# Performance work log

Measured on AMD Instinct MI355X. Metric: run time of the kernel, lower is better.

The kernel has to match this reference:

```python
import jax, jax.numpy as jnp
import numpy as np
import math

B = 262144
STATE = 6
TOTAL_MEAS = 27
HID = 256
INPUT_DIM = TOTAL_MEAS * 2 + 1 + STATE + 12  # 73
PI = math.pi
NORM_R_SCALE = 500.0 / 150000.0
ANG_IDX = np.array([0, 1, 3, 4, 6, 9, 10, 12, 13, 15, 18, 19, 21, 22, 24])
ANG_MASK = np.zeros((TOTAL_MEAS,), dtype=bool)
ANG_MASK[ANG_IDX] = True


def setup_inputs() -> dict:
    key = jax.random.key(0)
    ks = jax.random.split(key, 16)
    s = lambda fan: 1.0 / math.sqrt(fan)
    inp = {
        "meas": jax.random.normal(ks[0], (B, TOTAL_MEAS), jnp.float32),
        "mask": jnp.ones((B, TOTAL_MEAS), jnp.float32),
        "dt": jax.random.uniform(ks[1], (B,), jnp.float32),
        "baselines": jax.random.normal(ks[2], (B, 12), jnp.float32),
        "x_prev": jax.random.normal(ks[3], (B, STATE), jnp.float32),
        "hx": jnp.zeros((B, HID), jnp.float32),
        # GRU params (torch gate order: r, z, n)
        "W_ih": jax.random.uniform(ks[4], (3 * HID, INPUT_DIM), jnp.float32, -s(HID), s(HID)),
        "W_hh": jax.random.uniform(ks[5], (3 * HID, HID), jnp.float32, -s(HID), s(HID)),
        "b_ih": jax.random.uniform(ks[6], (3 * HID,), jnp.float32, -s(HID), s(HID)),
        "b_hh": jax.random.uniform(ks[7], (3 * HID,), jnp.float32, -s(HID), s(HID)),
        # LayerNorm
        "ln_g": jnp.ones((HID,), jnp.float32),
        "ln_b": jnp.zeros((HID,), jnp.float32),
        # MLP head: 256 -> 256 -> 128 -> 6*27
        "W1": jax.random.uniform(ks[8], (256, HID), jnp.float32, -s(HID), s(HID)),
        "b1": jax.random.uniform(ks[9], (256,), jnp.float32, -s(HID), s(HID)),
        "W2": jax.random.uniform(ks[10], (128, 256), jnp.float32, -s(256), s(256)),
        "b2": jax.random.uniform(ks[11], (128,), jnp.float32, -s(256), s(256)),
        "W3": jax.random.uniform(ks[12], (STATE * TOTAL_MEAS, 128), jnp.float32, -s(128), s(128)),
        "b3": jax.random.uniform(ks[13], (STATE * TOTAL_MEAS,), jnp.float32, -s(128), s(128)),
    }
    return inp


def _wrap_angle(a):
    two_pi = 2.0 * PI
    return a - two_pi * jnp.round(a / two_pi)


def _platform_y_pred(x_rel):
    # x_rel: [B, 6] -> [B, 9] radar/EO measurement
    r_xy = jnp.sqrt(x_rel[:, 0] ** 2 + x_rel[:, 2] ** 2 + 1e-9)
    az = jnp.arctan2(x_rel[:, 2], x_rel[:, 0]) / PI
    el = jnp.arctan2(x_rel[:, 4], r_xy) / PI
    r = jnp.sqrt(x_rel[:, 0] ** 2 + x_rel[:, 2] ** 2 + x_rel[:, 4] ** 2 + 1e-9)
    z = jnp.zeros_like(r)
    return jnp.stack([az, el, r, az, el, z, az, z, z], axis=1)


def _forward(meas, mask, dt, baselines, x_prev, hx,
             W_ih, W_hh, b_ih, b_hh, ln_g, ln_b, W1, b1, W2, b2, W3, b3):
    # f_predict (CV model): x0 += dt*x1, x2 += dt*x3, x4 += dt*x5
    dt_scaled = dt * NORM_R_SCALE  # [B]
    zcol = jnp.zeros_like(x_prev[:, :1])
    shift = jnp.concatenate([x_prev[:, 1:2], zcol, x_prev[:, 3:4], zcol, x_prev[:, 5:6], zcol], axis=1)
    x_minus = x_prev + dt_scaled[:, None] * shift  # [B, 6]

    y_pred = jnp.concatenate([
        _platform_y_pred(x_minus),
        _platform_y_pred(x_minus - baselines[:, 0:6]),
        _platform_y_pred(x_minus - baselines[:, 6:12]),
    ], axis=1)  # [B, 27]

    innov = meas - y_pred
    wrapped = _wrap_angle(innov * PI) / PI
    innov = jnp.where(jnp.asarray(ANG_MASK)[None, :], wrapped, innov)
    innov = innov * mask

    rnn_in = jnp.concatenate([innov, mask, dt[:, None], x_minus, baselines], axis=1)  # [B, 73]

    # single-step GRU (torch semantics, gate order r,z,n)
    gi = rnn_in @ W_ih.T + b_ih  # [B, 3H]
    gh = hx @ W_hh.T + b_hh      # [B, 3H]
    gi_r, gi_z, gi_n = jnp.split(gi, 3, axis=1)
    gh_r, gh_z, gh_n = jnp.split(gh, 3, axis=1)
    r = jax.nn.sigmoid(gi_r + gh_r)
    z = jax.nn.sigmoid(gi_z + gh_z)
    n = jnp.tanh(gi_n + r * gh_n)
    h_new = (1.0 - z) * n + z * hx  # [B, H]

    # LayerNorm
    mu = jnp.mean(h_new, axis=-1, keepdims=True)
    var = jnp.var(h_new, axis=-1, keepdims=True)
    h_ln = (h_new - mu) / jnp.sqrt(var + 1e-5) * ln_g + ln_b

    # MLP gain head (dropout inactive at inference)
    f1 = jax.nn.relu(h_ln @ W1.T + b1)
    f2 = jax.nn.relu(f1 @ W2.T + b2)
    K = (f2 @ W3.T + b3).reshape(-1, STATE, TOTAL_MEAS)
    K = jnp.clip(K, -3.0, 3.0)

    correction = jnp.einsum('bsm,bm->bs', K, innov)
    x_new = jnp.clip(x_minus + correction, -5.0, 5.0)
    return x_new, h_new


def reference(meas, mask, dt, baselines, x_prev, hx,
              W_ih, W_hh, b_ih, b_hh, ln_g, ln_b, W1, b1, W2, b2, W3, b3):
    return _forward(meas, mask, dt, baselines, x_prev, hx,
                    W_ih, W_hh, b_ih, b_hh, ln_g, ln_b, W1, b1, W2, b2, W3, b3)
```

## Files before the change

kernel.cpp:

```cpp
#include <hip/hip_runtime.h>
#include <math.h>

#define B_TOTAL  262144
#define ROWS     64
#define NWG      (B_TOTAL/ROWS)
#define NTHR     256
#define PI_F     3.14159265358979323846f
#define NORM_R   (500.0f/150000.0f)

typedef float  f32x4  __attribute__((ext_vector_type(4)));
typedef short  bf16x8 __attribute__((ext_vector_type(8)));

#define W_TOTAL (49*8192)

#define LDS_RB   0
#define LDS_HB   13312
#define LDS_STG  46080
#define LDS_XMC  78848
#define LDS_TOTAL 80384

#define WAIT_VM4  asm volatile("s_waitcnt vmcnt(4)" ::: "memory")
#define WAIT_VM0  asm volatile("s_waitcnt vmcnt(0)" ::: "memory")
#define WAIT_LGKM asm volatile("s_waitcnt lgkmcnt(0)" ::: "memory")
#define BARv      __builtin_amdgcn_s_barrier()

__device__ __forceinline__ ushort f2bf(float f){
    union { float f; unsigned u; } v; v.f = f;
    unsigned r = v.u + 0x7FFFu + ((v.u >> 16) & 1u);
    return (ushort)(r >> 16);
}
__device__ __forceinline__ float b2f(ushort u){
    union { unsigned u; float f; } v; v.u = ((unsigned)u) << 16;
    return v.f;
}
__device__ __forceinline__ unsigned pk2(float a, float b){
    return (unsigned)f2bf(a) | ((unsigned)f2bf(b) << 16);
}
__device__ __forceinline__ float upk(unsigned u, int hi){
    return b2f((ushort)(hi ? (u >> 16) : (u & 0xffffu)));
}
__device__ __forceinline__ float sigm(float x){ return 1.0f/(1.0f+__expf(-x)); }
__device__ __forceinline__ float tanh_(float x){ return 1.0f - 2.0f/(__expf(2.0f*x)+1.0f); }
__device__ __forceinline__ int swzb(int row, int k){
    return ((row<<9) + (k<<1)) ^ ((row&7)<<4);
}
__device__ __forceinline__ bf16x8 rdW(const char* gb, int col, int lk){
    int slot = lk ^ ((col >> 1) & 3);
    return *(const bf16x8*)(gb + col*64 + slot*16);
}
__device__ __forceinline__ void stage16(const ushort* src, char* dst, int w, int lane){
    #pragma unroll
    for (int i = 0; i < 4; ++i)
        __builtin_amdgcn_global_load_lds(
            (const __attribute__((address_space(1))) void*)(src + (size_t)((w*4+i)*64 + lane)*8),
            (__attribute__((address_space(3))) void*)(dst + (w*4+i)*1024),
            16, 0, 0);
}
#define PH(g) do { \
    if ((g) < 48) stage16(ws + (size_t)((g)+1)*8192, STG + (((g)+1)&1)*16384, w, lane); \
    if ((g) < 48) WAIT_VM4; else WAIT_VM0; \
    BARv; \
} while(0)

__device__ __forceinline__ void ldA4_rb(const ushort* Rbu, int lr, int kb, int lk8, bf16x8 a[4]){
    #pragma unroll
    for (int i = 0; i < 4; ++i)
        a[i] = *(const bf16x8*)(Rbu + (i*16 + lr)*104 + kb*32 + lk8);
}
__device__ __forceinline__ void ldA4_hb(const char* Hb, int lr, int kb, int lk8, bf16x8 a[4]){
    #pragma unroll
    for (int i = 0; i < 4; ++i)
        a[i] = *(const bf16x8*)(Hb + swzb(i*16 + lr, kb*32 + lk8));
}
__device__ __forceinline__ void mmW(const char* base, int colbase, int lr, int lk,
                                    const bf16x8 a[4], f32x4 acc[4][4]){
    #pragma unroll
    for (int j = 0; j < 4; ++j) {
        bf16x8 wf = rdW(base, colbase + j*16 + lr, lk);
        #pragma unroll
        for (int i = 0; i < 4; ++i)
            acc[i][j] = __builtin_amdgcn_mfma_f32_16x16x32_bf16(wf, a[i], acc[i][j], 0,0,0);
    }
}

__global__ void prep_weights(const float* __restrict__ W_ih, const float* __restrict__ W_hh,
                             const float* __restrict__ W1, const float* __restrict__ W2,
                             const float* __restrict__ W3, ushort* __restrict__ ws)
{
    int id = blockIdx.x*256 + threadIdx.x;
    if (id >= W_TOTAL) return;
    int g = id >> 13;
    int u = id & 8191;
    float v = 0.0f;
    if (g >= 41 && g < 45) {
        int half = u >> 12, u2 = u & 4095;
        int col = u2 >> 5, v5 = u2 & 31, slot = v5 >> 3, e = v5 & 7;
        int kq = slot ^ ((col >> 1) & 3);
        int kb = (g-41)*2 + half;
        v = W2[col*256 + kb*32 + kq*8 + e];
    } else {
        int col = u >> 5, v5 = u & 31, slot = v5 >> 3, e = v5 & 7;
        int kq = slot ^ ((col >> 1) & 3);
        if (g < 3) {
            int k = g*32 + kq*8 + e;
            if (k < 73) v = W_ih[(512+col)*73 + k];
        } else if (g < 11) {
            int k = (g-3)*32 + kq*8 + e;
            v = W_hh[(512+col)*256 + k];
        } else if (g < 22) {
            int k = (g-11)*32 + kq*8 + e;
            v = (k < 73) ? W_ih[col*73 + k] : ((k < 96) ? 0.0f : W_hh[col*256 + (k-96)]);
        } else if (g < 33) {
            int k = (g-22)*32 + kq*8 + e;
            v = (k < 73) ? W_ih[(256+col)*73 + k] : ((k < 96) ? 0.0f : W_hh[(256+col)*256 + (k-96)]);
        } else if (g < 41) {
            int k = (g-33)*32 + kq*8 + e;
            v = W1[col*256 + k];
        } else {
            int k = (g-45)*32 + kq*8 + e;
            if (col < 162) v = W3[col*128 + k];
        }
    }
    ws[id] = f2bf(v);
}

__global__ __launch_bounds__(NTHR, 2) void knet_mfma(
    const float* __restrict__ meas, const float* __restrict__ mask,
    const float* __restrict__ dt,   const float* __restrict__ baselines,
    const float* __restrict__ x_prev, const float* __restrict__ hx,
    const float* __restrict__ b_ih, const float* __restrict__ b_hh,
    const float* __restrict__ ln_g, const float* __restrict__ ln_b,
    const float* __restrict__ b1,   const float* __restrict__ b2,
    const float* __restrict__ b3,
    const ushort* __restrict__ ws,
    float* __restrict__ out)
{
    extern __shared__ char smem[];
    ushort* Rbu  = (ushort*)(smem + LDS_RB);
    char*   Hb   = smem + LDS_HB;
    char*   STG  = smem + LDS_STG;
    float*  xmc  = (float*)(smem + LDS_XMC);

    const int tid  = threadIdx.x;
    const int w    = __builtin_amdgcn_readfirstlane(tid >> 6);
    const int nq   = w;
    const int lane = tid & 63;
    const int lr   = lane & 15;
    const int lk   = lane >> 4;
    const int lk8  = lk * 8;
    const int row0 = blockIdx.x * ROWS;
    float* hout = out + (size_t)B_TOTAL*6;

    stage16(ws, STG, w, lane);

    float* scr = (float*)Hb;
    {
        const size_t m0 = (size_t)row0*27;
        for (int i = tid; i < 1728; i += NTHR) scr[i]        = meas[m0 + i];
        for (int i = tid; i < 1728; i += NTHR) scr[1728 + i] = mask[m0 + i];
        for (int i = tid; i < 768;  i += NTHR) scr[3456 + i] = baselines[(size_t)row0*12 + i];
        for (int i = tid; i < 384;  i += NTHR) scr[4224 + i] = x_prev[(size_t)row0*6 + i];
        if (tid < 64) scr[4608 + tid] = dt[row0 + tid];
    }
    __syncthreads();

    {
        const int row = lane;
        const float dtv = scr[4608 + row];
        const float dts = dtv * NORM_R;
        float xp[6], xm[6];
        #pragma unroll
        for (int s = 0; s < 6; ++s) xp[s] = scr[4224 + row*6 + s];
        xm[0] = xp[0] + dts*xp[1]; xm[1] = xp[1];
        xm[2] = xp[2] + dts*xp[3]; xm[3] = xp[3];
        xm[4] = xp[4] + dts*xp[5]; xm[5] = xp[5];
        if (w < 3) {
            float xr[6];
            #pragma unroll
            for (int s = 0; s < 6; ++s) {
                float b = (w == 0) ? 0.0f : scr[3456 + row*12 + (w-1)*6 + s];
                xr[s] = xm[s] - b;
            }
            float rxy = sqrtf(xr[0]*xr[0] + xr[2]*xr[2] + 1e-9f);
            float azv = atan2f(xr[2], xr[0]) * (1.0f/PI_F);
            float elv = atan2f(xr[4], rxy)   * (1.0f/PI_F);
            float rrv = sqrtf(xr[0]*xr[0] + xr[2]*xr[2] + xr[4]*xr[4] + 1e-9f);
            float y[9] = {azv, elv, rrv, azv, elv, 0.0f, azv, 0.0f, 0.0f};
            const bool ang[9] = {true,true,false,true,true,false,true,false,false};
            #pragma unroll
            for (int i = 0; i < 9; ++i) {
                int m = w*9 + i;
                float ms = scr[1728 + row*27 + m];
                float v  = scr[row*27 + m] - y[i];
                if (ang[i]) v = v - 2.0f*rintf(v*0.5f);
                v *= ms;
                Rbu[row*104 + m]      = f2bf(v);
                Rbu[row*104 + 27 + m] = f2bf(ms);
            }
        } else {
            Rbu[row*104 + 54] = f2bf(dtv);
            #pragma unroll
            for (int s = 0; s < 6; ++s) Rbu[row*104 + 55 + s] = f2bf(xm[s]);
            #pragma unroll
            for (int q = 0; q < 12; ++q) Rbu[row*104 + 61 + q] = f2bf(scr[3456 + row*12 + q]);
            #pragma unroll
            for (int k = 73; k < 96; ++k) Rbu[row*104 + k] = 0;
            #pragma unroll
            for (int s = 0; s < 6; ++s) xmc[row*6 + s] = xm[s];
        }
    }
    __syncthreads();

    {
        const size_t hbase = (size_t)row0 * 256;
        #pragma unroll
        for (int ii = 0; ii < 8; ++ii) {
            int cid = tid + ii*NTHR;
            int r  = cid >> 5;
            int k0 = (cid & 31) << 3;
            const float4* p = (const float4*)(hx + hbase + (size_t)r*256 + k0);
            float4 u = p[0], v2 = p[1];
            bf16x8 o;
            o[0]=(short)f2bf(u.x);  o[1]=(short)f2bf(u.y);  o[2]=(short)f2bf(u.z);  o[3]=(short)f2bf(u.w);
            o[4]=(short)f2bf(v2.x); o[5]=(short)f2bf(v2.y); o[6]=(short)f2bf(v2.z); o[7]=(short)f2bf(v2.w);
            *(bf16x8*)(Hb + swzb(r, k0)) = o;
        }
    }
    __syncthreads();

    unsigned ginp[4][2], ghnp[4][2], npk[4][2];
    unsigned ginq[4][4][2], ghnq[4][4][2];

    {
        f32x4 acc[4][4];
        #pragma unroll
        for (int i = 0; i < 4; ++i)
            #pragma unroll
            for (int j = 0; j < 4; ++j) acc[i][j] = (f32x4){0,0,0,0};
        #pragma unroll
        for (int p = 0; p < 3; ++p) {
            PH(p);
            bf16x8 a[4];
            ldA4_rb(Rbu, lr, p, lk8, a);
            __builtin_amdgcn_s_setprio(1);
            mmW(STG + (p&1)*16384, nq*64, lr, lk, a, acc);
            __builtin_amdgcn_s_setprio(0);
            BARv;
        }
        #pragma unroll
        for (int j = 0; j < 4; ++j) {
            const int c0 = nq*64 + j*16 + lk*4;
            f32x4 b4 = *(const f32x4*)(b_ih + 512 + c0);
            #pragma unroll
            for (int i = 0; i < 4; ++i) {
                ginq[i][j][0] = pk2(acc[i][j][0] + b4[0], acc[i][j][1] + b4[1]);
                ginq[i][j][1] = pk2(acc[i][j][2] + b4[2], acc[i][j][3] + b4[3]);
            }
        }
    }
    {
        f32x4 acc[4][4];
        #pragma unroll
        for (int i = 0; i < 4; ++i)
            #pragma unroll
            for (int j = 0; j < 4; ++j) acc[i][j] = (f32x4){0,0,0,0};
        #pragma unroll
        for (int p = 0; p < 8; ++p) {
            PH(3+p);
            bf16x8 a[4];
            ldA4_hb(Hb, lr, p, lk8, a);
            __builtin_amdgcn_s_setprio(1);
            mmW(STG + ((3+p)&1)*16384, nq*64, lr, lk, a, acc);
            __builtin_amdgcn_s_setprio(0);
            BARv;
        }
        #pragma unroll
        for (int j = 0; j < 4; ++j) {
            const int c0 = nq*64 + j*16 + lk*4;
            f32x4 b4 = *(const f32x4*)(b_hh + 512 + c0);
            #pragma unroll
            for (int i = 0; i < 4; ++i) {
                ghnq[i][j][0] = pk2(acc[i][j][0] + b4[0], acc[i][j][1] + b4[1]);
                ghnq[i][j][1] = pk2(acc[i][j][2] + b4[2], acc[i][j][3] + b4[3]);
            }
        }
    }
    unsigned nq_[4][4][2];
    {
        f32x4 acc[4][4];
        #pragma unroll
        for (int i = 0; i < 4; ++i)
            #pragma unroll
            for (int j = 0; j < 4; ++j) acc[i][j] = (f32x4){0,0,0,0};
        #pragma unroll
        for (int p = 0; p < 11; ++p) {
            PH(11+p);
            bf16x8 a[4];
            if (p < 3) ldA4_rb(Rbu, lr, p, lk8, a);
            else       ldA4_hb(Hb, lr, p-3, lk8, a);
            __builtin_amdgcn_s_setprio(1);
            mmW(STG + ((11+p)&1)*16384, nq*64, lr, lk, a, acc);
            __builtin_amdgcn_s_setprio(0);
            BARv;
        }
        #pragma unroll
        for (int j = 0; j < 4; ++j) {
            const int c0 = nq*64 + j*16 + lk*4;
            f32x4 bi4 = *(const f32x4*)(b_ih + c0);
            f32x4 bh4 = *(const f32x4*)(b_hh + c0);
            #pragma unroll
            for (int i = 0; i < 4; ++i) {
                float nv[4];
                #pragma unroll
                for (int e = 0; e < 4; ++e) {
                    float rg = sigm(acc[i][j][e] + bi4[e] + bh4[e]);
                    nv[e] = tanh_(upk(ginq[i][j][e>>1], e&1) + rg*upk(ghnq[i][j][e>>1], e&1));
                }
                nq_[i][j][0] = pk2(nv[0], nv[1]);
                nq_[i][j][1] = pk2(nv[2], nv[3]);
            }
        }
    }
    {
        f32x4 acc[4][4];
        #pragma unroll
        for (int i = 0; i < 4; ++i)
            #pragma unroll
            for (int j = 0; j < 4; ++j) acc[i][j] = (f32x4){0,0,0,0};
        #pragma unroll
        for (int p = 0; p < 11; ++p) {
            PH(22+p);
            bf16x8 a[4];
            if (p < 3) ldA4_rb(Rbu, lr, p, lk8, a);
            else       ldA4_hb(Hb, lr, p-3, lk8, a);
            __builtin_amdgcn_s_setprio(1);
            mmW(STG + ((22+p)&1)*16384, nq*64, lr, lk, a, acc);
            __builtin_amdgcn_s_setprio(0);
            BARv;
        }
        #pragma unroll
        for (int j = 0; j < 4; ++j) {
            const int c0 = nq*64 + j*16 + lk*4;
            f32x4 bi4 = *(const f32x4*)(b_ih + 256 + c0);
            f32x4 bh4 = *(const f32x4*)(b_hh + 256 + c0);
            #pragma unroll
            for (int i = 0; i < 4; ++i) {
                const int row = i*16 + lr;
                uint2 hxd = *(const uint2*)(Hb + swzb(row, c0));
                float hn4[4];
                #pragma unroll
                for (int e = 0; e < 4; ++e) {
                    float zg = sigm(acc[i][j][e] + bi4[e] + bh4[e]);
                    float hxv = upk(e < 2 ? hxd.x : hxd.y, e&1);
                    hn4[e] = (1.0f - zg)*upk(nq_[i][j][e>>1], e&1) + zg*hxv;
                }
                uint2 o; o.x = pk2(hn4[0], hn4[1]); o.y = pk2(hn4[2], hn4[3]);
                *(uint2*)(Hb + swzb(row, c0)) = o;
                float4 st = { hn4[0], hn4[1], hn4[2], hn4[3] };
                *(float4*)(hout + (size_t)(row0+row)*256 + c0) = st;
            }
        }
    }
    WAIT_LGKM; BARv;

    {
        const int row = tid >> 2;
        const int o   = tid & 3;
        bf16x8 ch[8];
        float sum = 0.0f, sq = 0.0f;
        #pragma unroll
        for (int jx = 0; jx < 8; ++jx) {
            ch[jx] = *(const bf16x8*)(Hb + swzb(row, o*64 + jx*8));
            #pragma unroll
            for (int e = 0; e < 8; ++e) {
                float f = b2f((ushort)ch[jx][e]);
                sum += f; sq += f*f;
            }
        }
        sum += __shfl_xor(sum, 1); sum += __shfl_xor(sum, 2);
        sq  += __shfl_xor(sq, 1);  sq  += __shfl_xor(sq, 2);
        float mu   = sum * (1.0f/256.0f);
        float rstd = rsqrtf(sq*(1.0f/256.0f) - mu*mu + 1e-5f);
        #pragma unroll
        for (int jx = 0; jx < 8; ++jx) {
            int col0 = o*64 + jx*8;
            float4 g0 = *(const float4*)(ln_g + col0), g1 = *(const float4*)(ln_g + col0 + 4);
            float4 bb0 = *(const float4*)(ln_b + col0), bb1 = *(const float4*)(ln_b + col0 + 4);
            bf16x8 oo;
            oo[0] = (short)f2bf((b2f((ushort)ch[jx][0]) - mu)*rstd*g0.x + bb0.x);
            oo[1] = (short)f2bf((b2f((ushort)ch[jx][1]) - mu)*rstd*g0.y + bb0.y);
            oo[2] = (short)f2bf((b2f((ushort)ch[jx][2]) - mu)*rstd*g0.z + bb0.z);
            oo[3] = (short)f2bf((b2f((ushort)ch[jx][3]) - mu)*rstd*g0.w + bb0.w);
            oo[4] = (short)f2bf((b2f((ushort)ch[jx][4]) - mu)*rstd*g1.x + bb1.x);
            oo[5] = (short)f2bf((b2f((ushort)ch[jx][5]) - mu)*rstd*g1.y + bb1.y);
            oo[6] = (short)f2bf((b2f((ushort)ch[jx][6]) - mu)*rstd*g1.z + bb1.z);
            oo[7] = (short)f2bf((b2f((ushort)ch[jx][7]) - mu)*rstd*g1.w + bb1.w);
            *(bf16x8*)(Hb + swzb(row, col0)) = oo;
        }
    }
    WAIT_LGKM; BARv;

    {
        f32x4 acc[4][4];
        #pragma unroll
        for (int i = 0; i < 4; ++i)
            #pragma unroll
            for (int j = 0; j < 4; ++j) acc[i][j] = (f32x4){0,0,0,0};
        #pragma unroll
        for (int p = 0; p < 8; ++p) {
            PH(33+p);
            bf16x8 a[4];
            ldA4_hb(Hb, lr, p, lk8, a);
            __builtin_amdgcn_s_setprio(1);
            mmW(STG + ((33+p)&1)*16384, nq*64, lr, lk, a, acc);
            __builtin_amdgcn_s_setprio(0);
            BARv;
        }
        #pragma unroll
        for (int j = 0; j < 4; ++j) {
            const int c0 = nq*64 + j*16 + lk*4;
            f32x4 b4 = *(const f32x4*)(b1 + c0);
            #pragma unroll
            for (int i = 0; i < 4; ++i) {
                const int row = i*16 + lr;
                uint2 o;
                o.x = pk2(fmaxf(acc[i][j][0]+b4[0],0.f), fmaxf(acc[i][j][1]+b4[1],0.f));
                o.y = pk2(fmaxf(acc[i][j][2]+b4[2],0.f), fmaxf(acc[i][j][3]+b4[3],0.f));
                *(uint2*)(Hb + swzb(row, c0)) = o;
            }
        }
    }
    WAIT_LGKM; BARv;

    f32x4 c3[4][2];
    #pragma unroll
    for (int i = 0; i < 4; ++i)
        #pragma unroll
        for (int j = 0; j < 2; ++j) c3[i][j] = (f32x4){0,0,0,0};
    #pragma unroll
    for (int p = 0; p < 4; ++p) {
        PH(41+p);
        const char* sb = STG + ((41+p)&1)*16384;
        #pragma unroll
        for (int h = 0; h < 2; ++h) {
            bf16x8 a[4];
            ldA4_hb(Hb, lr, 2*p + h, lk8, a);
            __builtin_amdgcn_s_setprio(1);
            #pragma unroll
            for (int j = 0; j < 2; ++j) {
                bf16x8 wf = rdW(sb + h*8192, nq*32 + j*16 + lr, lk);
                #pragma unroll
                for (int i = 0; i < 4; ++i)
                    c3[i][j] = __builtin_amdgcn_mfma_f32_16x16x32_bf16(wf, a[i], c3[i][j], 0,0,0);
            }
            __builtin_amdgcn_s_setprio(0);
        }
        BARv;
    }
    ushort* F2 = (ushort*)Hb;
    #pragma unroll
    for (int j = 0; j < 2; ++j) {
        const int c0 = nq*32 + j*16 + lk*4;
        f32x4 b4 = *(const f32x4*)(b2 + c0);
        #pragma unroll
        for (int i = 0; i < 4; ++i) {
            const int row = i*16 + lr;
            uint2 o;
            o.x = pk2(fmaxf(c3[i][j][0]+b4[0],0.f), fmaxf(c3[i][j][1]+b4[1],0.f));
            o.y = pk2(fmaxf(c3[i][j][2]+b4[2],0.f), fmaxf(c3[i][j][3]+b4[3],0.f));
            *(uint2*)((char*)F2 + row*272 + c0*2) = o;
        }
    }
    WAIT_LGKM; BARv;

    {
        f32x4 c4[4][3];
        #pragma unroll
        for (int i = 0; i < 4; ++i)
            #pragma unroll
            for (int j = 0; j < 3; ++j) c4[i][j] = (f32x4){0,0,0,0};
        #pragma unroll
        for (int p = 0; p < 4; ++p) {
            PH(45+p);
            const char* sb = STG + ((45+p)&1)*16384;
            bf16x8 a[4];
            #pragma unroll
            for (int i = 0; i < 4; ++i)
                a[i] = *(const bf16x8*)((const char*)F2 + (i*16 + lr)*272 + (p*32 + lk8)*2);
            __builtin_amdgcn_s_setprio(1);
            #pragma unroll
            for (int j = 0; j < 3; ++j) {
                bf16x8 wf = rdW(sb, nq*48 + j*16 + lr, lk);
                #pragma unroll
                for (int i = 0; i < 4; ++i)
                    c4[i][j] = __builtin_amdgcn_mfma_f32_16x16x32_bf16(wf, a[i], c4[i][j], 0,0,0);
            }
            __builtin_amdgcn_s_setprio(0);
            BARv;
        }
        #pragma unroll
        for (int j = 0; j < 3; ++j)
            #pragma unroll
            for (int i = 0; i < 4; ++i) {
                const int row = i*16 + lr;
                #pragma unroll
                for (int e = 0; e < 4; ++e) {
                    int col = nq*48 + j*16 + lk*4 + e;
                    if (col < 162) {
                        int s = col / 27, m = col - s*27;
                        float K = fminf(fmaxf(c4[i][j][e] + b3[col], -3.0f), 3.0f);
                        atomicAdd(&xmc[row*6 + s], K * b2f(Rbu[row*104 + m]));
                    }
                }
            }
    }
    __syncthreads();

    for (int t = tid; t < ROWS*6; t += NTHR) {
        int row = t / 6, s = t - row*6;
        float v = fminf(fmaxf(xmc[t], -5.0f), 5.0f);
        out[(size_t)(row0+row)*6 + s] = v;
    }
}

extern "C" void kernel_launch(void* const* d_in, const int* in_sizes, int n_in,
                              void* d_out, int out_size, void* d_ws, size_t ws_size,
                              hipStream_t stream) {
    const float* meas      = (const float*)d_in[0];
    const float* mask      = (const float*)d_in[1];
    const float* dtv       = (const float*)d_in[2];
    const float* baselines = (const float*)d_in[3];
    const float* x_prev    = (const float*)d_in[4];
    const float* hx        = (const float*)d_in[5];
    const float* W_ih      = (const float*)d_in[6];
    const float* W_hh      = (const float*)d_in[7];
    const float* b_ih      = (const float*)d_in[8];
    const float* b_hh      = (const float*)d_in[9];
    const float* ln_g      = (const float*)d_in[10];
    const float* ln_b      = (const float*)d_in[11];
    const float* W1        = (const float*)d_in[12];
    const float* b1        = (const float*)d_in[13];
    const float* W2        = (const float*)d_in[14];
    const float* b2        = (const float*)d_in[15];
    const float* W3        = (const float*)d_in[16];
    const float* b3        = (const float*)d_in[17];
    ushort* wsb = (ushort*)d_ws;
    float* outp = (float*)d_out;

    prep_weights<<<(W_TOTAL + 255)/256, 256, 0, stream>>>(W_ih, W_hh, W1, W2, W3, wsb);
    knet_mfma<<<NWG, NTHR, LDS_TOTAL, stream>>>(
        meas, mask, dtv, baselines, x_prev, hx,
        b_ih, b_hh, ln_g, ln_b, b1, b2, b3, wsb, outp);
}
```

Baseline: 701.8 us.

## Use 8 waves with per-wave private weight rings and fused GRU gate GEMMs

Doubles the workgroup to 512 threads. Each wave now owns a 32-column slice and keeps its own double-buffered weight ring in LDS, prefetched two k-blocks ahead with async global-to-LDS loads, which removes the workgroup barriers from every k-step. The r, z and n gate GEMMs are fused into a single pass over the concatenated input and hidden state, with the input-side n part captured after k-block 2. This drops the separate per-gate passes. LDS use grows to about 146 KB, which likely cuts occupancy to one workgroup per CU, and the larger register footprint is a risk.

```diff
diff --git a/kernel.cpp b/kernel.cpp
--- a/kernel.cpp
+++ b/kernel.cpp
@@ -4,7 +4,7 @@
 #define B_TOTAL  262144
 #define ROWS     64
 #define NWG      (B_TOTAL/ROWS)
-#define NTHR     256
+#define NTHR     512
 #define PI_F     3.14159265358979323846f
 #define NORM_R   (500.0f/150000.0f)
 
@@ -15,14 +15,15 @@
 
 #define LDS_RB   0
 #define LDS_HB   13312
-#define LDS_STG  46080
-#define LDS_XMC  78848
-#define LDS_TOTAL 80384
-
-#define WAIT_VM4  asm volatile("s_waitcnt vmcnt(4)" ::: "memory")
+#define LDS_RING 46080
+#define LDS_XMC  144384
+#define LDS_TOTAL 145920
+
+#define WAIT_VM6  asm volatile("s_waitcnt vmcnt(6)" ::: "memory")
+#define WAIT_VM2  asm volatile("s_waitcnt vmcnt(2)" ::: "memory")
+#define WAIT_VM1  asm volatile("s_waitcnt vmcnt(1)" ::: "memory")
 #define WAIT_VM0  asm volatile("s_waitcnt vmcnt(0)" ::: "memory")
 #define WAIT_LGKM asm volatile("s_waitcnt lgkmcnt(0)" ::: "memory")
-#define BARv      __builtin_amdgcn_s_barrier()
 
 __device__ __forceinline__ ushort f2bf(float f){
     union { float f; unsigned u; } v; v.f = f;
@@ -44,23 +45,24 @@
 __device__ __forceinline__ int swzb(int row, int k){
     return ((row<<9) + (k<<1)) ^ ((row&7)<<4);
 }
-__device__ __forceinline__ bf16x8 rdW(const char* gb, int col, int lk){
-    int slot = lk ^ ((col >> 1) & 3);
-    return *(const bf16x8*)(gb + col*64 + slot*16);
-}
-__device__ __forceinline__ void stage16(const ushort* src, char* dst, int w, int lane){
-    #pragma unroll
-    for (int i = 0; i < 4; ++i)
+__device__ __forceinline__ bf16x8 rdW2(const char* chunk, int cl, int lk){
+    int slot = lk ^ ((cl >> 1) & 3);
+    return *(const bf16x8*)(chunk + cl*64 + slot*16);
+}
+__device__ __forceinline__ void stage2k(const ushort* src, char* dst, int lane){
+    #pragma unroll
+    for (int i = 0; i < 2; ++i)
         __builtin_amdgcn_global_load_lds(
-            (const __attribute__((address_space(1))) void*)(src + (size_t)((w*4+i)*64 + lane)*8),
-            (__attribute__((address_space(3))) void*)(dst + (w*4+i)*1024),
+            (const __attribute__((address_space(1))) void*)(src + i*512 + lane*8),
+            (__attribute__((address_space(3))) void*)(dst + i*1024),
             16, 0, 0);
 }
-#define PH(g) do { \
-    if ((g) < 48) stage16(ws + (size_t)((g)+1)*8192, STG + (((g)+1)&1)*16384, w, lane); \
-    if ((g) < 48) WAIT_VM4; else WAIT_VM0; \
-    BARv; \
-} while(0)
+__device__ __forceinline__ void stage1k(const ushort* src, char* dst, int lane){
+    __builtin_amdgcn_global_load_lds(
+        (const __attribute__((address_space(1))) void*)(src + lane*8),
+        (__attribute__((address_space(3))) void*)(dst),
+        16, 0, 0);
+}
 
 __device__ __forceinline__ void ldA4_rb(const ushort* Rbu, int lr, int kb, int lk8, bf16x8 a[4]){
     #pragma unroll
@@ -71,16 +73,6 @@
     #pragma unroll
     for (int i = 0; i < 4; ++i)
         a[i] = *(const bf16x8*)(Hb + swzb(i*16 + lr, kb*32 + lk8));
-}
-__device__ __forceinline__ void mmW(const char* base, int colbase, int lr, int lk,
-                                    const bf16x8 a[4], f32x4 acc[4][4]){
-    #pragma unroll
-    for (int j = 0; j < 4; ++j) {
-        bf16x8 wf = rdW(base, colbase + j*16 + lr, lk);
-        #pragma unroll
-        for (int i = 0; i < 4; ++i)
-            acc[i][j] = __builtin_amdgcn_mfma_f32_16x16x32_bf16(wf, a[i], acc[i][j], 0,0,0);
-    }
 }
 
 __global__ void prep_weights(const float* __restrict__ W_ih, const float* __restrict__ W_hh,
@@ -138,20 +130,27 @@
     extern __shared__ char smem[];
     ushort* Rbu  = (ushort*)(smem + LDS_RB);
     char*   Hb   = smem + LDS_HB;
-    char*   STG  = smem + LDS_STG;
     float*  xmc  = (float*)(smem + LDS_XMC);
 
     const int tid  = threadIdx.x;
     const int w    = __builtin_amdgcn_readfirstlane(tid >> 6);
-    const int nq   = w;
     const int lane = tid & 63;
     const int lr   = lane & 15;
     const int lk   = lane >> 4;
     const int lk8  = lk * 8;
+    const int cw   = w * 32;
     const int row0 = blockIdx.x * ROWS;
+    char* ring = smem + LDS_RING + w*12288;
     float* hout = out + (size_t)B_TOTAL*6;
 
-    stage16(ws, STG, w, lane);
+    auto issue_triple = [&](int kb, char* buf){
+        stage2k(ws + (size_t)(11+kb)*8192 + w*1024, buf,        lane);
+        stage2k(ws + (size_t)(22+kb)*8192 + w*1024, buf + 2048, lane);
+        stage2k(ws + (size_t)kb*8192      + w*1024, buf + 4096, lane);
+    };
+
+    issue_triple(0, ring);
+    issue_triple(1, ring + 6144);
 
     float* scr = (float*)Hb;
     {
@@ -164,7 +163,7 @@
     }
     __syncthreads();
 
-    {
+    if (w < 4) {
         const int row = lane;
         const float dtv = scr[4608 + row];
         const float dts = dtv * NORM_R;
@@ -214,7 +213,7 @@
     {
         const size_t hbase = (size_t)row0 * 256;
         #pragma unroll
-        for (int ii = 0; ii < 8; ++ii) {
+        for (int ii = 0; ii < 4; ++ii) {
             int cid = tid + ii*NTHR;
             int r  = cid >> 5;
             int k0 = (cid & 31) << 3;
@@ -228,162 +227,106 @@
     }
     __syncthreads();
 
-    unsigned ginp[4][2], ghnp[4][2], npk[4][2];
-    unsigned ginq[4][4][2], ghnq[4][4][2];
+    f32x4 ar[4][2], az[4][2], ag[4][2];
+    unsigned gipk[4][2][2];
+    #pragma unroll
+    for (int i = 0; i < 4; ++i)
+        #pragma unroll
+        for (int j = 0; j < 2; ++j) { ar[i][j]=(f32x4){0,0,0,0}; az[i][j]=(f32x4){0,0,0,0}; ag[i][j]=(f32x4){0,0,0,0}; }
+
+    #pragma unroll
+    for (int kb = 0; kb < 11; ++kb) {
+        if (kb == 10)     WAIT_VM0;
+        else if (kb > 0)  WAIT_VM6;
+        bf16x8 a[4];
+        if (kb < 3) ldA4_rb(Rbu, lr, kb, lk8, a);
+        else        ldA4_hb(Hb, lr, kb-3, lk8, a);
+        const char* bb = ring + (kb&1)*6144;
+        bf16x8 br[2], bz[2], bg[2];
+        #pragma unroll
+        for (int j = 0; j < 2; ++j) {
+            br[j] = rdW2(bb,        j*16 + lr, lk);
+            bz[j] = rdW2(bb + 2048, j*16 + lr, lk);
+            bg[j] = rdW2(bb + 4096, j*16 + lr, lk);
+        }
+        WAIT_LGKM;
+        if (kb + 2 <= 10) issue_triple(kb+2, ring + (kb&1)*6144);
+        __builtin_amdgcn_s_setprio(1);
+        #pragma unroll
+        for (int j = 0; j < 2; ++j)
+            #pragma unroll
+            for (int i = 0; i < 4; ++i) {
+                ar[i][j] = __builtin_amdgcn_mfma_f32_16x16x32_bf16(br[j], a[i], ar[i][j], 0,0,0);
+                az[i][j] = __builtin_amdgcn_mfma_f32_16x16x32_bf16(bz[j], a[i], az[i][j], 0,0,0);
+                ag[i][j] = __builtin_amdgcn_mfma_f32_16x16x32_bf16(bg[j], a[i], ag[i][j], 0,0,0);
+            }
+        __builtin_amdgcn_s_setprio(0);
+        if (kb == 2) {
+            #pragma unroll
+            for (int j = 0; j < 2; ++j) {
+                const int c0 = cw + j*16 + lk*4;
+                f32x4 b4 = *(const f32x4*)(b_ih + 512 + c0);
+                #pragma unroll
+                for (int i = 0; i < 4; ++i) {
+                    gipk[i][j][0] = pk2(ag[i][j][0] + b4[0], ag[i][j][1] + b4[1]);
+                    gipk[i][j][1] = pk2(ag[i][j][2] + b4[2], ag[i][j][3] + b4[3]);
+                    ag[i][j] = (f32x4){0,0,0,0};
+                }
+            }
+        }
+    }
+    __syncthreads();
+
+    #pragma unroll
+    for (int j = 0; j < 2; ++j) {
+        const int c0 = cw + j*16 + lk*4;
+        f32x4 bir = *(const f32x4*)(b_ih + c0),       bhr = *(const f32x4*)(b_hh + c0);
+        f32x4 biz = *(const f32x4*)(b_ih + 256 + c0), bhz = *(const f32x4*)(b_hh + 256 + c0);
+        f32x4 bhn = *(const f32x4*)(b_hh + 512 + c0);
+        #pragma unroll
+        for (int i = 0; i < 4; ++i) {
+            const int row = i*16 + lr;
+            uint2 hxd = *(const uint2*)(Hb + swzb(row, c0));
+            float hn4[4];
+            #pragma unroll
+            for (int e = 0; e < 4; ++e) {
+                float rg = sigm(ar[i][j][e] + bir[e] + bhr[e]);
+                float zg = sigm(az[i][j][e] + biz[e] + bhz[e]);
+                float ng = tanh_(upk(gipk[i][j][e>>1], e&1) + rg*(ag[i][j][e] + bhn[e]));
+                float hxv = upk(e < 2 ? hxd.x : hxd.y, e&1);
+                hn4[e] = (1.0f - zg)*ng + zg*hxv;
+            }
+            uint2 o; o.x = pk2(hn4[0], hn4[1]); o.y = pk2(hn4[2], hn4[3]);
+            *(uint2*)(Hb + swzb(row, c0)) = o;
+            float4 st = { hn4[0], hn4[1], hn4[2], hn4[3] };
+            *(float4*)(hout + (size_t)(row0+row)*256 + c0) = st;
+        }
+    }
+    stage2k(ws + (size_t)33*8192 + w*1024, ring,        lane);
+    stage2k(ws + (size_t)34*8192 + w*1024, ring + 2048, lane);
+    __syncthreads();
 
     {
-        f32x4 acc[4][4];
-        #pragma unroll
-        for (int i = 0; i < 4; ++i)
-            #pragma unroll
-            for (int j = 0; j < 4; ++j) acc[i][j] = (f32x4){0,0,0,0};
-        #pragma unroll
-        for (int p = 0; p < 3; ++p) {
-            PH(p);
-            bf16x8 a[4];
-            ldA4_rb(Rbu, lr, p, lk8, a);
-            __builtin_amdgcn_s_setprio(1);
-            mmW(STG + (p&1)*16384, nq*64, lr, lk, a, acc);
-            __builtin_amdgcn_s_setprio(0);
-            BARv;
-        }
-        #pragma unroll
-        for (int j = 0; j < 4; ++j) {
-            const int c0 = nq*64 + j*16 + lk*4;
-            f32x4 b4 = *(const f32x4*)(b_ih + 512 + c0);
-            #pragma unroll
-            for (int i = 0; i < 4; ++i) {
-                ginq[i][j][0] = pk2(acc[i][j][0] + b4[0], acc[i][j][1] + b4[1]);
-                ginq[i][j][1] = pk2(acc[i][j][2] + b4[2], acc[i][j][3] + b4[3]);
-            }
-        }
-    }
-    {
-        f32x4 acc[4][4];
-        #pragma unroll
-        for (int i = 0; i < 4; ++i)
-            #pragma unroll
-            for (int j = 0; j < 4; ++j) acc[i][j] = (f32x4){0,0,0,0};
-        #pragma unroll
-        for (int p = 0; p < 8; ++p) {
-            PH(3+p);
-            bf16x8 a[4];
-            ldA4_hb(Hb, lr, p, lk8, a);
-            __builtin_amdgcn_s_setprio(1);
-            mmW(STG + ((3+p)&1)*16384, nq*64, lr, lk, a, acc);
-            __builtin_amdgcn_s_setprio(0);
-            BARv;
-        }
-        #pragma unroll
-        for (int j = 0; j < 4; ++j) {
-            const int c0 = nq*64 + j*16 + lk*4;
-            f32x4 b4 = *(const f32x4*)(b_hh + 512 + c0);
-            #pragma unroll
-            for (int i = 0; i < 4; ++i) {
-                ghnq[i][j][0] = pk2(acc[i][j][0] + b4[0], acc[i][j][1] + b4[1]);
-                ghnq[i][j][1] = pk2(acc[i][j][2] + b4[2], acc[i][j][3] + b4[3]);
-            }
-        }
-    }
-    unsigned nq_[4][4][2];
-    {
-        f32x4 acc[4][4];
-        #pragma unroll
-        for (int i = 0; i < 4; ++i)
-            #pragma unroll
-            for (int j = 0; j < 4; ++j) acc[i][j] = (f32x4){0,0,0,0};
-        #pragma unroll
-        for (int p = 0; p < 11; ++p) {
-            PH(11+p);
-            bf16x8 a[4];
-            if (p < 3) ldA4_rb(Rbu, lr, p, lk8, a);
-            else       ldA4_hb(Hb, lr, p-3, lk8, a);
-            __builtin_amdgcn_s_setprio(1);
-            mmW(STG + ((11+p)&1)*16384, nq*64, lr, lk, a, acc);
-            __builtin_amdgcn_s_setprio(0);
-            BARv;
-        }
-        #pragma unroll
-        for (int j = 0; j < 4; ++j) {
-            const int c0 = nq*64 + j*16 + lk*4;
-            f32x4 bi4 = *(const f32x4*)(b_ih + c0);
-            f32x4 bh4 = *(const f32x4*)(b_hh + c0);
-            #pragma unroll
-            for (int i = 0; i < 4; ++i) {
-                float nv[4];
-                #pragma unroll
-                for (int e = 0; e < 4; ++e) {
-                    float rg = sigm(acc[i][j][e] + bi4[e] + bh4[e]);
-                    nv[e] = tanh_(upk(ginq[i][j][e>>1], e&1) + rg*upk(ghnq[i][j][e>>1], e&1));
-                }
-                nq_[i][j][0] = pk2(nv[0], nv[1]);
-                nq_[i][j][1] = pk2(nv[2], nv[3]);
-            }
-        }
-    }
-    {
-        f32x4 acc[4][4];
-        #pragma unroll
-        for (int i = 0; i < 4; ++i)
-            #pragma unroll
-            for (int j = 0; j < 4; ++j) acc[i][j] = (f32x4){0,0,0,0};
-        #pragma unroll
-        for (int p = 0; p < 11; ++p) {
-            PH(22+p);
-            bf16x8 a[4];
-            if (p < 3) ldA4_rb(Rbu, lr, p, lk8, a);
-            else       ldA4_hb(Hb, lr, p-3, lk8, a);
-            __builtin_amdgcn_s_setprio(1);
-            mmW(STG + ((22+p)&1)*16384, nq*64, lr, lk, a, acc);
-            __builtin_amdgcn_s_setprio(0);
-            BARv;
-        }
-        #pragma unroll
-        for (int j = 0; j < 4; ++j) {
-            const int c0 = nq*64 + j*16 + lk*4;
-            f32x4 bi4 = *(const f32x4*)(b_ih + 256 + c0);
-            f32x4 bh4 = *(const f32x4*)(b_hh + 256 + c0);
-            #pragma unroll
-            for (int i = 0; i < 4; ++i) {
-                const int row = i*16 + lr;
-                uint2 hxd = *(const uint2*)(Hb + swzb(row, c0));
-                float hn4[4];
-                #pragma unroll
-                for (int e = 0; e < 4; ++e) {
-                    float zg = sigm(acc[i][j][e] + bi4[e] + bh4[e]);
-                    float hxv = upk(e < 2 ? hxd.x : hxd.y, e&1);
-                    hn4[e] = (1.0f - zg)*upk(nq_[i][j][e>>1], e&1) + zg*hxv;
-                }
-                uint2 o; o.x = pk2(hn4[0], hn4[1]); o.y = pk2(hn4[2], hn4[3]);
-                *(uint2*)(Hb + swzb(row, c0)) = o;
-                float4 st = { hn4[0], hn4[1], hn4[2], hn4[3] };
-                *(float4*)(hout + (size_t)(row0+row)*256 + c0) = st;
-            }
-        }
-    }
-    WAIT_LGKM; BARv;
-
-    {
-        const int row = tid >> 2;
-        const int o   = tid & 3;
-        bf16x8 ch[8];
+        const int row = tid >> 3;
+        const int o   = tid & 7;
+        bf16x8 ch[4];
         float sum = 0.0f, sq = 0.0f;
         #pragma unroll
-        for (int jx = 0; jx < 8; ++jx) {
-            ch[jx] = *(const bf16x8*)(Hb + swzb(row, o*64 + jx*8));
+        for (int jx = 0; jx < 4; ++jx) {
+            ch[jx] = *(const bf16x8*)(Hb + swzb(row, o*32 + jx*8));
             #pragma unroll
             for (int e = 0; e < 8; ++e) {
                 float f = b2f((ushort)ch[jx][e]);
                 sum += f; sq += f*f;
             }
         }
-        sum += __shfl_xor(sum, 1); sum += __shfl_xor(sum, 2);
-        sq  += __shfl_xor(sq, 1);  sq  += __shfl_xor(sq, 2);
+        sum += __shfl_xor(sum, 1); sum += __shfl_xor(sum, 2); sum += __shfl_xor(sum, 4);
+        sq  += __shfl_xor(sq, 1);  sq  += __shfl_xor(sq, 2);  sq  += __shfl_xor(sq, 4);
         float mu   = sum * (1.0f/256.0f);
         float rstd = rsqrtf(sq*(1.0f/256.0f) - mu*mu + 1e-5f);
         #pragma unroll
-        for (int jx = 0; jx < 8; ++jx) {
-            int col0 = o*64 + jx*8;
+        for (int jx = 0; jx < 4; ++jx) {
+            int col0 = o*32 + jx*8;
             float4 g0 = *(const float4*)(ln_g + col0), g1 = *(const float4*)(ln_g + col0 + 4);
             float4 bb0 = *(const float4*)(ln_b + col0), bb1 = *(const float4*)(ln_b + col0 + 4);
             bf16x8 oo;
@@ -398,114 +341,126 @@
             *(bf16x8*)(Hb + swzb(row, col0)) = oo;
         }
     }
-    WAIT_LGKM; BARv;
-
-    {
-        f32x4 acc[4][4];
-        #pragma unroll
-        for (int i = 0; i < 4; ++i)
-            #pragma unroll
-            for (int j = 0; j < 4; ++j) acc[i][j] = (f32x4){0,0,0,0};
-        #pragma unroll
-        for (int p = 0; p < 8; ++p) {
-            PH(33+p);
-            bf16x8 a[4];
-            ldA4_hb(Hb, lr, p, lk8, a);
-            __builtin_amdgcn_s_setprio(1);
-            mmW(STG + ((33+p)&1)*16384, nq*64, lr, lk, a, acc);
-            __builtin_amdgcn_s_setprio(0);
-            BARv;
-        }
-        #pragma unroll
-        for (int j = 0; j < 4; ++j) {
-            const int c0 = nq*64 + j*16 + lk*4;
-            f32x4 b4 = *(const f32x4*)(b1 + c0);
-            #pragma unroll
-            for (int i = 0; i < 4; ++i) {
-                const int row = i*16 + lr;
-                uint2 o;
-                o.x = pk2(fmaxf(acc[i][j][0]+b4[0],0.f), fmaxf(acc[i][j][1]+b4[1],0.f));
-                o.y = pk2(fmaxf(acc[i][j][2]+b4[2],0.f), fmaxf(acc[i][j][3]+b4[3],0.f));
-                *(uint2*)(Hb + swzb(row, c0)) = o;
-            }
-        }
-    }
-    WAIT_LGKM; BARv;
-
-    f32x4 c3[4][2];
+    __syncthreads();
+
+    f32x4 c2[4][2];
     #pragma unroll
     for (int i = 0; i < 4; ++i)
         #pragma unroll
-        for (int j = 0; j < 2; ++j) c3[i][j] = (f32x4){0,0,0,0};
-    #pragma unroll
-    for (int p = 0; p < 4; ++p) {
-        PH(41+p);
-        const char* sb = STG + ((41+p)&1)*16384;
-        #pragma unroll
-        for (int h = 0; h < 2; ++h) {
-            bf16x8 a[4];
-            ldA4_hb(Hb, lr, 2*p + h, lk8, a);
-            __builtin_amdgcn_s_setprio(1);
-            #pragma unroll
-            for (int j = 0; j < 2; ++j) {
-                bf16x8 wf = rdW(sb + h*8192, nq*32 + j*16 + lr, lk);
-                #pragma unroll
-                for (int i = 0; i < 4; ++i)
-                    c3[i][j] = __builtin_amdgcn_mfma_f32_16x16x32_bf16(wf, a[i], c3[i][j], 0,0,0);
-            }
-            __builtin_amdgcn_s_setprio(0);
-        }
-        BARv;
-    }
-    ushort* F2 = (ushort*)Hb;
+        for (int j = 0; j < 2; ++j) c2[i][j] = (f32x4){0,0,0,0};
+    #pragma unroll
+    for (int kb = 0; kb < 8; ++kb) {
+        if (kb == 7)     WAIT_VM0;
+        else if (kb > 0) WAIT_VM2;
+        bf16x8 a[4];
+        ldA4_hb(Hb, lr, kb, lk8, a);
+        const char* bb = ring + (kb&1)*2048;
+        bf16x8 b[2];
+        #pragma unroll
+        for (int j = 0; j < 2; ++j) b[j] = rdW2(bb, j*16 + lr, lk);
+        WAIT_LGKM;
+        if (kb + 2 <= 7) stage2k(ws + (size_t)(33+kb+2)*8192 + w*1024, ring + (kb&1)*2048, lane);
+        __builtin_amdgcn_s_setprio(1);
+        #pragma unroll
+        for (int j = 0; j < 2; ++j)
+            #pragma unroll
+            for (int i = 0; i < 4; ++i)
+                c2[i][j] = __builtin_amdgcn_mfma_f32_16x16x32_bf16(b[j], a[i], c2[i][j], 0,0,0);
+        __builtin_amdgcn_s_setprio(0);
+    }
+    stage1k(ws + (size_t)41*8192 + 0*4096 + w*512, ring,        lane);
+    stage1k(ws + (size_t)41*8192 + 1*4096 + w*512, ring + 1024, lane);
+    __syncthreads();
     #pragma unroll
     for (int j = 0; j < 2; ++j) {
-        const int c0 = nq*32 + j*16 + lk*4;
-        f32x4 b4 = *(const f32x4*)(b2 + c0);
+        const int c0 = cw + j*16 + lk*4;
+        f32x4 b4 = *(const f32x4*)(b1 + c0);
         #pragma unroll
         for (int i = 0; i < 4; ++i) {
             const int row = i*16 + lr;
             uint2 o;
-            o.x = pk2(fmaxf(c3[i][j][0]+b4[0],0.f), fmaxf(c3[i][j][1]+b4[1],0.f));
-            o.y = pk2(fmaxf(c3[i][j][2]+b4[2],0.f), fmaxf(c3[i][j][3]+b4[3],0.f));
+            o.x = pk2(fmaxf(c2[i][j][0]+b4[0],0.f), fmaxf(c2[i][j][1]+b4[1],0.f));
+            o.y = pk2(fmaxf(c2[i][j][2]+b4[2],0.f), fmaxf(c2[i][j][3]+b4[3],0.f));
+            *(uint2*)(Hb + swzb(row, c0)) = o;
+        }
+    }
+    __syncthreads();
+
+    f32x4 c3[4];
+    #pragma unroll
+    for (int i = 0; i < 4; ++i) c3[i] = (f32x4){0,0,0,0};
+    #pragma unroll
+    for (int kb = 0; kb < 8; ++kb) {
+        if (kb == 7)     WAIT_VM0;
+        else if (kb > 0) WAIT_VM1;
+        bf16x8 a[4];
+        ldA4_hb(Hb, lr, kb, lk8, a);
+        bf16x8 b = rdW2(ring + (kb&1)*1024, lr, lk);
+        WAIT_LGKM;
+        if (kb + 2 <= 7) {
+            int k2 = kb + 2;
+            stage1k(ws + (size_t)(41 + (k2>>1))*8192 + (k2&1)*4096 + w*512, ring + (kb&1)*1024, lane);
+        }
+        __builtin_amdgcn_s_setprio(1);
+        #pragma unroll
+        for (int i = 0; i < 4; ++i)
+            c3[i] = __builtin_amdgcn_mfma_f32_16x16x32_bf16(b, a[i], c3[i], 0,0,0);
+        __builtin_amdgcn_s_setprio(0);
+    }
+    stage2k(ws + (size_t)45*8192 + w*1024, ring,        lane);
+    stage2k(ws + (size_t)46*8192 + w*1024, ring + 2048, lane);
+    __syncthreads();
+    ushort* F2 = (ushort*)Hb;
+    {
+        const int c0 = w*16 + lk*4;
+        f32x4 b4 = *(const f32x4*)(b2 + c0);
+        #pragma unroll
+        for (int i = 0; i < 4; ++i) {
+            const int row = i*16 + lr;
+            uint2 o;
+            o.x = pk2(fmaxf(c3[i][0]+b4[0],0.f), fmaxf(c3[i][1]+b4[1],0.f));
+            o.y = pk2(fmaxf(c3[i][2]+b4[2],0.f), fmaxf(c3[i][3]+b4[3],0.f));
             *(uint2*)((char*)F2 + row*272 + c0*2) = o;
         }
     }
-    WAIT_LGKM; BARv;
+    __syncthreads();
 
     {
-        f32x4 c4[4][3];
+        f32x4 c4[4][2];
         #pragma unroll
         for (int i = 0; i < 4; ++i)
             #pragma unroll
-            for (int j = 0; j < 3; ++j) c4[i][j] = (f32x4){0,0,0,0};
-        #pragma unroll
-        for (int p = 0; p < 4; ++p) {
-            PH(45+p);
-            const char* sb = STG + ((45+p)&1)*16384;
+            for (int j = 0; j < 2; ++j) c4[i][j] = (f32x4){0,0,0,0};
+        #pragma unroll
+        for (int kb = 0; kb < 4; ++kb) {
+            if (kb == 3)     WAIT_VM0;
+            else if (kb > 0) WAIT_VM2;
             bf16x8 a[4];
             #pragma unroll
             for (int i = 0; i < 4; ++i)
-                a[i] = *(const bf16x8*)((const char*)F2 + (i*16 + lr)*272 + (p*32 + lk8)*2);
+                a[i] = *(const bf16x8*)((const char*)F2 + (i*16 + lr)*272 + (kb*32 + lk8)*2);
+            const char* bb = ring + (kb&1)*2048;
+            bf16x8 b[2];
+            #pragma unroll
+            for (int j = 0; j < 2; ++j) b[j] = rdW2(bb, j*16 + lr, lk);
+            WAIT_LGKM;
+            if (kb + 2 <= 3) stage2k(ws + (size_t)(45+kb+2)*8192 + w*1024, ring + (kb&1)*2048, lane);
             __builtin_amdgcn_s_setprio(1);
             #pragma unroll
-            for (int j = 0; j < 3; ++j) {
-                bf16x8 wf = rdW(sb, nq*48 + j*16 + lr, lk);
+            for (int j = 0; j < 2; ++j)
                 #pragma unroll
                 for (int i = 0; i < 4; ++i)
-                    c4[i][j] = __builtin_amdgcn_mfma_f32_16x16x32_bf16(wf, a[i], c4[i][j], 0,0,0);
-            }
+                    c4[i][j] = __builtin_amdgcn_mfma_f32_16x16x32_bf16(b[j], a[i], c4[i][j], 0,0,0);
             __builtin_amdgcn_s_setprio(0);
-            BARv;
-        }
-        #pragma unroll
-        for (int j = 0; j < 3; ++j)
+        }
+        #pragma unroll
+        for (int j = 0; j < 2; ++j)
             #pragma unroll
             for (int i = 0; i < 4; ++i) {
                 const int row = i*16 + lr;
                 #pragma unroll
                 for (int e = 0; e < 4; ++e) {
-                    int col = nq*48 + j*16 + lk*4 + e;
+                    int col = cw + j*16 + lk*4 + e;
                     if (col < 162) {
                         int s = col / 27, m = col - s*27;
                         float K = fminf(fmaxf(c4[i][j][e] + b3[col], -3.0f), 3.0f);
```

New measurement: 743.4 us. 5.9% more time.
